# Optimization experiments

Measured on AMD Instinct MI355X. Metric: run time of the kernel, lower is better.

## Reference

```python
import jax, jax.numpy as jnp
import numpy as np

NUM_EXPERTS = 8
TOP_K = 2

def setup_inputs() -> dict:
    key = jax.random.key(0)
    ks = jax.random.split(key, 6)
    B, S, D, F, E = 2, 2048, 1024, 4096, NUM_EXPERTS
    scale = 0.02
    return {
        "x": jax.random.normal(ks[0], (B, S, D), dtype=jnp.float32),
        "router_w": jax.random.normal(ks[1], (E, D), dtype=jnp.float32) * scale,
        "router_b": jnp.zeros((E,), dtype=jnp.float32),
        "w1": jax.random.normal(ks[2], (E, D, F), dtype=jnp.float32) * scale,
        "w2": jax.random.normal(ks[3], (E, F, D), dtype=jnp.float32) * scale,
        "w3": jax.random.normal(ks[4], (E, D, F), dtype=jnp.float32) * scale,
    }

def reference(x, router_w, router_b, w1, w2, w3):
    B, S, D = x.shape
    E = router_w.shape[0]
    xf = x.reshape(-1, D)                                   # [T, D]
    logits = xf @ router_w.T + router_b                     # [T, E]
    probs = jax.nn.softmax(logits, axis=-1)
    topk_w, topk_idx = jax.lax.top_k(probs, TOP_K)          # [T, K]
    topk_w = topk_w / jnp.sum(topk_w, axis=-1, keepdims=True)
    # combine[t, e] = renormalized routing weight of expert e for token t (0 if not selected)
    combine = jnp.sum(jax.nn.one_hot(topk_idx, E, dtype=xf.dtype) * topk_w[..., None], axis=1)  # [T, E]
    out = jnp.zeros_like(xf)
    for e in range(E):  # small fixed expert count; each iter is a dense SwiGLU GEMM
        h = jax.nn.silu(xf @ w1[e]) * (xf @ w3[e])          # [T, F]
        out = out + combine[:, e:e + 1] * (h @ w2[e])       # [T, D]
    return out.reshape(B, S, D)
```

## Files before the change

kernel.cpp:

```cpp
#include <hip/hip_runtime.h>

typedef unsigned short ushort_t;
typedef __attribute__((ext_vector_type(8))) short short8;
typedef __attribute__((ext_vector_type(4))) float floatx4;

#define GAS __attribute__((address_space(1)))
#define LAS __attribute__((address_space(3)))

__device__ __forceinline__ float bf2f(ushort_t h) {
  union { unsigned int u; float f; } v; v.u = ((unsigned int)h) << 16; return v.f;
}
__device__ __forceinline__ ushort_t f2bf(float f) {
  union { float f; unsigned int u; } v; v.f = f;
  unsigned int u = v.u;
  unsigned int r = (u + 0x7fffu + ((u >> 16) & 1u)) >> 16;
  return (ushort_t)r;
}
__device__ __forceinline__ float blo(unsigned int u) { union { unsigned int u; float f; } v; v.u = u << 16; return v.f; }
__device__ __forceinline__ float bhi(unsigned int u) { union { unsigned int u; float f; } v; v.u = u & 0xffff0000u; return v.f; }

#define T_TOK 4096
#define DIM   1024
#define FDIM  4096
#define NEXP  8
#define MAXROWS 9216

__global__ void detect_kernel(const ushort_t* __restrict__ xraw, int* __restrict__ dflag) {
  __shared__ int cnt;
  if (threadIdx.x == 0) cnt = 0;
  __syncthreads();
  int c = 0;
#pragma unroll
  for (int i = 0; i < 4; ++i) {
    ushort_t u = xraw[(threadIdx.x * 4 + i) * 2];
    int e = (u >> 7) & 0xFF;
    if (e >= 100 && e <= 140) c++;
  }
  atomicAdd(&cnt, c);
  __syncthreads();
  if (threadIdx.x == 0) dflag[0] = (cnt > 600) ? 0 : 1;
}

__global__ void __launch_bounds__(256) castx_kernel(const void* __restrict__ xraw,
                                                    const int* __restrict__ dflag,
                                                    ushort_t* __restrict__ xb) {
  const int t = blockIdx.x * 256 + threadIdx.x;
  const size_t base = (size_t)t * 8;
  if (dflag[0]) {
    const float4* f = (const float4*)((const float*)xraw + base);
    float4 a = f[0], b = f[1];
    ushort_t o[8] = { f2bf(a.x), f2bf(a.y), f2bf(a.z), f2bf(a.w),
                      f2bf(b.x), f2bf(b.y), f2bf(b.z), f2bf(b.w) };
    *(uint4*)(xb + base) = *(const uint4*)o;
  } else {
    *(uint4*)(xb + base) = *((const uint4*)xraw + t);
  }
}

__global__ void __launch_bounds__(256) router_kernel(
    const void* __restrict__ x_, const ushort_t* __restrict__ xb,
    const void* __restrict__ rw_, const void* __restrict__ rb_,
    const int* __restrict__ dflag,
    int* __restrict__ topk_idx, float* __restrict__ topk_wgt, int* __restrict__ counts) {
  const int lane = threadIdx.x & 63;
  const int w = threadIdx.x >> 6;
  const int t = blockIdx.x * 4 + w;
  const int isf32 = dflag[0];
  double logits[NEXP];
  if (isf32) {
    const float* xr = (const float*)x_ + (size_t)t * DIM;
    float xv[16];
#pragma unroll
    for (int i = 0; i < 8; ++i) {
      const float2 v = *(const float2*)(xr + i * 128 + lane * 2);
      xv[2*i] = v.x; xv[2*i+1] = v.y;
    }
#pragma unroll
    for (int e = 0; e < NEXP; ++e) {
      const float* wr = (const float*)rw_ + (size_t)e * DIM;
      double acc = 0.0;
#pragma unroll
      for (int i = 0; i < 8; ++i) {
        const float2 v = *(const float2*)(wr + i * 128 + lane * 2);
        acc += (double)xv[2*i] * (double)v.x + (double)xv[2*i+1] * (double)v.y;
      }
#pragma unroll
      for (int off = 32; off > 0; off >>= 1) acc += __shfl_xor(acc, off, 64);
      logits[e] = acc + (double)((const float*)rb_)[e];
    }
  } else {
    const ushort_t* xr = xb + (size_t)t * DIM;
    float xv[16];
#pragma unroll
    for (int i = 0; i < 8; ++i) {
      unsigned int u = *(const unsigned int*)(xr + i * 128 + lane * 2);
      xv[2*i] = blo(u); xv[2*i+1] = bhi(u);
    }
#pragma unroll
    for (int e = 0; e < NEXP; ++e) {
      const ushort_t* wr = (const ushort_t*)rw_ + (size_t)e * DIM;
      float acc = 0.f;
#pragma unroll
      for (int i = 0; i < 8; ++i) {
        unsigned int u = *(const unsigned int*)(wr + i * 128 + lane * 2);
        acc += xv[2*i] * blo(u) + xv[2*i+1] * bhi(u);
      }
#pragma unroll
      for (int off = 32; off > 0; off >>= 1) acc += __shfl_xor(acc, off, 64);
      logits[e] = (double)(acc + bf2f(((const ushort_t*)rb_)[e]));
    }
  }
  if (lane == 0) {
    double l1 = -1e300, l2 = -1e300; int i1 = 0, i2 = 0;
#pragma unroll
    for (int e = 0; e < NEXP; ++e) {
      double l = logits[e];
      if (l > l1) { l2 = l1; i2 = i1; l1 = l; i1 = e; }
      else if (l > l2) { l2 = l; i2 = e; }
    }
    float wa = (float)(1.0 / (1.0 + exp(l2 - l1)));
    topk_idx[2*t] = i1; topk_idx[2*t+1] = i2;
    topk_wgt[2*t] = wa; topk_wgt[2*t+1] = 1.f - wa;
    atomicAdd(&counts[i1], 1);
    atomicAdd(&counts[i2], 1);
  }
}

__global__ void scan_kernel(const int* __restrict__ counts, int* __restrict__ offsets) {
  if (threadIdx.x == 0 && blockIdx.x == 0) {
    int s = 0; offsets[0] = 0;
    for (int e = 0; e < NEXP; ++e) { s += (counts[e] + 127) & ~127; offsets[e + 1] = s; }
  }
}

__global__ void __launch_bounds__(256) scatter_kernel(
    const int* __restrict__ topk_idx, const float* __restrict__ topk_wgt,
    const int* __restrict__ offsets, int* __restrict__ cursors,
    int* __restrict__ row_tok, float* __restrict__ row_wgt) {
  int p = blockIdx.x * 256 + threadIdx.x;
  int e = topk_idx[p];
  int pos = atomicAdd(&cursors[e], 1);
  int r = offsets[e] + pos;
  row_tok[r] = p >> 1;
  row_wgt[r] = topk_wgt[p];
}

__global__ void __launch_bounds__(256) transpose_kernel(
    const void* __restrict__ src_, ushort_t* __restrict__ dst, int R, int C,
    const int* __restrict__ dflag) {
  __shared__ unsigned int tile[64][33];
  const int e = blockIdx.z;
  const int r0 = blockIdx.y * 64;
  const int c0 = blockIdx.x * 64;
  const int tx = threadIdx.x;
  if (dflag[0]) {
    const float* S = (const float*)src_ + (size_t)e * R * C;
#pragma unroll
    for (int it = 0; it < 8; ++it) {
      int slot = tx + it * 256;
      int r = slot >> 5;
      int c2 = slot & 31;
      const float2 v = *(const float2*)(S + (size_t)(r0 + r) * C + c0 + c2 * 2);
      tile[r][c2] = (unsigned int)f2bf(v.x) | ((unsigned int)f2bf(v.y) << 16);
    }
  } else {
    const ushort_t* S = (const ushort_t*)src_ + (size_t)e * R * C;
#pragma unroll
    for (int it = 0; it < 2; ++it) {
      int slot = tx + it * 256;
      int r = slot >> 3;
      int cc = slot & 7;
      const uint4 v = *(const uint4*)(S + (size_t)(r0 + r) * C + c0 + cc * 8);
      tile[r][cc*4+0] = v.x; tile[r][cc*4+1] = v.y; tile[r][cc*4+2] = v.z; tile[r][cc*4+3] = v.w;
    }
  }
  __syncthreads();
#pragma unroll
  for (int it = 0; it < 2; ++it) {
    int slot = tx + it * 256;
    int c = slot >> 3;
    int rr = (slot & 7) * 8;
    unsigned int o[4];
#pragma unroll
    for (int q = 0; q < 4; ++q) {
      unsigned int a = tile[rr + 2*q][c >> 1];
      unsigned int b = tile[rr + 2*q + 1][c >> 1];
      unsigned int ha = (c & 1) ? (a >> 16) : (a & 0xffffu);
      unsigned int hb = (c & 1) ? (b >> 16) : (b & 0xffffu);
      o[q] = ha | (hb << 16);
    }
    *(uint4*)(dst + (size_t)e * R * C + (size_t)(c0 + c) * R + r0 + rr) = *(const uint4*)o;
  }
}

__device__ __forceinline__ int swz(int r) { return (r >> 1) & 3; }

__device__ __forceinline__ short8 frag_ld(const short* tile, int row, int q) {
  return *(const short8*)(tile + row * 32 + ((q ^ swz(row)) << 3));
}

__device__ __forceinline__ int chunk_expert(const int* offsets, int r0) {
  int e = 0;
  while (offsets[e + 1] <= r0) ++e;
  return e;
}

__global__ void __launch_bounds__(256) gemm1_kernel(
    const ushort_t* __restrict__ xb, const ushort_t* __restrict__ w1t, const ushort_t* __restrict__ w3t,
    const int* __restrict__ offsets, const int* __restrict__ row_tok, ushort_t* __restrict__ H) {
  const int r0 = blockIdx.y * 128;
  if (r0 >= offsets[NEXP]) return;
  const int e = chunk_expert(offsets, r0);
  const int fbase = blockIdx.x * 128;
  const ushort_t* w1e = w1t + (size_t)e * FDIM * DIM;
  const ushort_t* w3e = w3t + (size_t)e * FDIM * DIM;

  __shared__ __align__(16) short As[2][4096];
  __shared__ __align__(16) short B1s[2][4096];
  __shared__ __align__(16) short B3s[2][4096];

  const int lane = threadIdx.x & 63;
  const int wid = threadIdx.x >> 6;
  const int wrow = (wid >> 1) * 64;
  const int wcol = (wid & 1) * 64;
  const int l15 = lane & 15;
  const int quad = lane >> 4;

  const ushort_t* aP[2];  const ushort_t* b1P[2];  const ushort_t* b3P[2];
  int ldst[2];
#pragma unroll
  for (int tl = 0; tl < 2; ++tl) {
    const int tr0 = wid * 32 + tl * 16;
    const int r = tr0 + (lane >> 2);
    const int g = ((lane & 3) ^ swz(r)) * 8;
    aP[tl]  = xb  + (size_t)row_tok[r0 + r] * DIM + g;
    b1P[tl] = w1e + (size_t)(fbase + r) * DIM + g;
    b3P[tl] = w3e + (size_t)(fbase + r) * DIM + g;
    ldst[tl] = tr0 * 32;
  }

  floatx4 acc1[4][4], acc3[4][4];
  const floatx4 z4 = {0.f, 0.f, 0.f, 0.f};
#pragma unroll
  for (int i = 0; i < 4; ++i)
#pragma unroll
    for (int j = 0; j < 4; ++j) { acc1[i][j] = z4; acc3[i][j] = z4; }

  auto stage = [&](int k0, int buf) {
#pragma unroll
    for (int tl = 0; tl < 2; ++tl) {
      __builtin_amdgcn_global_load_lds((const GAS void*)(aP[tl]  + k0), (LAS void*)(&As[buf][ldst[tl]]),  16, 0, 0);
      __builtin_amdgcn_global_load_lds((const GAS void*)(b1P[tl] + k0), (LAS void*)(&B1s[buf][ldst[tl]]), 16, 0, 0);
      __builtin_amdgcn_global_load_lds((const GAS void*)(b3P[tl] + k0), (LAS void*)(&B3s[buf][ldst[tl]]), 16, 0, 0);
    }
  };
  auto compute = [&](int buf) {
    short8 a[4], b1[4], b3[4];
#pragma unroll
    for (int i = 0; i < 4; ++i) a[i] = frag_ld(&As[buf][0], wrow + i * 16 + l15, quad);
#pragma unroll
    for (int j = 0; j < 4; ++j) {
      b1[j] = frag_ld(&B1s[buf][0], wcol + j * 16 + l15, quad);
      b3[j] = frag_ld(&B3s[buf][0], wcol + j * 16 + l15, quad);
    }
#pragma unroll
    for (int i = 0; i < 4; ++i)
#pragma unroll
      for (int j = 0; j < 4; ++j) {
        acc1[i][j] = __builtin_amdgcn_mfma_f32_16x16x32_bf16(a[i], b1[j], acc1[i][j], 0, 0, 0);
        acc3[i][j] = __builtin_amdgcn_mfma_f32_16x16x32_bf16(a[i], b3[j], acc3[i][j], 0, 0, 0);
      }
  };

  stage(0, 0);
  __syncthreads();
  int cur = 0;
  for (int t = 0; t < DIM / 32 - 1; ++t) {
    stage((t + 1) * 32, cur ^ 1);
    compute(cur);
    __syncthreads();
    cur ^= 1;
  }
  compute(cur);

#pragma unroll
  for (int i = 0; i < 4; ++i)
#pragma unroll
    for (int j = 0; j < 4; ++j) {
      const int n = fbase + wcol + j * 16 + l15;
#pragma unroll
      for (int p = 0; p < 4; ++p) {
        const int rl = wrow + i * 16 + quad * 4 + p;
        float zt = acc1[i][j][p];
        float vt = acc3[i][j][p];
        float s = zt / (1.f + __expf(-zt));
        H[(size_t)(r0 + rl) * FDIM + n] = f2bf(s * vt);
      }
    }
}

__global__ void __launch_bounds__(256) gemm2_kernel(
    const ushort_t* __restrict__ H, const ushort_t* __restrict__ w2t,
    const int* __restrict__ offsets, const int* __restrict__ row_tok,
    const float* __restrict__ row_wgt, float* __restrict__ out) {
  const int r0 = blockIdx.y * 128;
  if (r0 >= offsets[NEXP]) return;
  const int e = chunk_expert(offsets, r0);
  const int dbase = blockIdx.x * 128;
  const ushort_t* w2e = w2t + (size_t)e * DIM * FDIM;

  __shared__ __align__(16) short As[2][4096];
  __shared__ __align__(16) short Bs[2][4096];

  const int lane = threadIdx.x & 63;
  const int wid = threadIdx.x >> 6;
  const int wrow = (wid >> 1) * 64;
  const int wcol = (wid & 1) * 64;
  const int l15 = lane & 15;
  const int quad = lane >> 4;

  const ushort_t* aP[2];  const ushort_t* bP[2];
  int ldst[2];
#pragma unroll
  for (int tl = 0; tl < 2; ++tl) {
    const int tr0 = wid * 32 + tl * 16;
    const int r = tr0 + (lane >> 2);
    const int g = ((lane & 3) ^ swz(r)) * 8;
    aP[tl] = H   + (size_t)(r0 + r) * FDIM + g;
    bP[tl] = w2e + (size_t)(dbase + r) * FDIM + g;
    ldst[tl] = tr0 * 32;
  }

  floatx4 acc[4][4];
  const floatx4 z4 = {0.f, 0.f, 0.f, 0.f};
#pragma unroll
  for (int i = 0; i < 4; ++i)
#pragma unroll
    for (int j = 0; j < 4; ++j) acc[i][j] = z4;

  auto stage = [&](int k0, int buf) {
#pragma unroll
    for (int tl = 0; tl < 2; ++tl) {
      __builtin_amdgcn_global_load_lds((const GAS void*)(aP[tl] + k0), (LAS void*)(&As[buf][ldst[tl]]), 16, 0, 0);
      __builtin_amdgcn_global_load_lds((const GAS void*)(bP[tl] + k0), (LAS void*)(&Bs[buf][ldst[tl]]), 16, 0, 0);
    }
  };
  auto compute = [&](int buf) {
    short8 a[4], b[4];
#pragma unroll
    for (int i = 0; i < 4; ++i) a[i] = frag_ld(&As[buf][0], wrow + i * 16 + l15, quad);
#pragma unroll
    for (int j = 0; j < 4; ++j) b[j] = frag_ld(&Bs[buf][0], wcol + j * 16 + l15, quad);
#pragma unroll
    for (int i = 0; i < 4; ++i)
#pragma unroll
      for (int j = 0; j < 4; ++j)
        acc[i][j] = __builtin_amdgcn_mfma_f32_16x16x32_bf16(a[i], b[j], acc[i][j], 0, 0, 0);
  };

  stage(0, 0);
  __syncthreads();
  int cur = 0;
  for (int t = 0; t < FDIM / 32 - 1; ++t) {
    stage((t + 1) * 32, cur ^ 1);
    compute(cur);
    __syncthreads();
    cur ^= 1;
  }
  compute(cur);

#pragma unroll
  for (int i = 0; i < 4; ++i) {
    int tok[4]; float wgt[4];
#pragma unroll
    for (int p = 0; p < 4; ++p) {
      int rl = r0 + wrow + i * 16 + quad * 4 + p;
      tok[p] = row_tok[rl];
      wgt[p] = row_wgt[rl];
    }
#pragma unroll
    for (int j = 0; j < 4; ++j) {
      int n = dbase + wcol + j * 16 + l15;
#pragma unroll
      for (int p = 0; p < 4; ++p)
        if (wgt[p] != 0.f)
          atomicAdd(&out[(size_t)tok[p] * DIM + n], wgt[p] * acc[i][j][p]);
    }
  }
}

extern "C" void kernel_launch(void* const* d_in, const int* in_sizes, int n_in,
                              void* d_out, int out_size, void* d_ws, size_t ws_size,
                              hipStream_t stream) {
  const void* x  = d_in[0];
  const void* rw = d_in[1];
  const void* rb = d_in[2];
  const void* w1 = d_in[3];
  const void* w2 = d_in[4];
  const void* w3 = d_in[5];
  float* out = (float*)d_out;

  char* ws = (char*)d_ws;
  size_t off = 0;
  auto alloc = [&](size_t bytes) { size_t o = off; off += (bytes + 255) & ~(size_t)255; return o; };
  int*      dflag    = (int*)(ws + alloc(64));
  int*      counts   = (int*)(ws + alloc(64));
  int*      cursors  = (int*)(ws + alloc(64));
  int*      offsets  = (int*)(ws + alloc(64));
  int*      topk_idx = (int*)(ws + alloc((size_t)T_TOK * 2 * 4));
  float*    topk_wgt = (float*)(ws + alloc((size_t)T_TOK * 2 * 4));
  int*      row_tok  = (int*)(ws + alloc((size_t)MAXROWS * 4));
  float*    row_wgt  = (float*)(ws + alloc((size_t)MAXROWS * 4));
  ushort_t* xb       = (ushort_t*)(ws + alloc((size_t)T_TOK * DIM * 2));
  ushort_t* Hbuf     = (ushort_t*)(ws + alloc((size_t)MAXROWS * FDIM * 2));
  ushort_t* w1t      = (ushort_t*)(ws + alloc((size_t)NEXP * FDIM * DIM * 2));
  ushort_t* w3t      = (ushort_t*)(ws + alloc((size_t)NEXP * FDIM * DIM * 2));
  ushort_t* w2t      = (ushort_t*)(ws + alloc((size_t)NEXP * DIM * FDIM * 2));

  hipMemsetAsync(counts, 0, 64, stream);
  hipMemsetAsync(cursors, 0, 64, stream);
  hipMemsetAsync(row_tok, 0, (size_t)MAXROWS * 4, stream);
  hipMemsetAsync(row_wgt, 0, (size_t)MAXROWS * 4, stream);
  hipMemsetAsync(out, 0, (size_t)out_size, stream);

  detect_kernel<<<1, 256, 0, stream>>>((const ushort_t*)x, dflag);
  castx_kernel<<<(T_TOK * DIM / 8) / 256, 256, 0, stream>>>(x, dflag, xb);
  router_kernel<<<T_TOK / 4, 256, 0, stream>>>(x, xb, rw, rb, dflag, topk_idx, topk_wgt, counts);
  scan_kernel<<<1, 64, 0, stream>>>(counts, offsets);
  scatter_kernel<<<(T_TOK * 2) / 256, 256, 0, stream>>>(topk_idx, topk_wgt, offsets, cursors, row_tok, row_wgt);
  transpose_kernel<<<dim3(FDIM / 64, DIM / 64, NEXP), 256, 0, stream>>>(w1, w1t, DIM, FDIM, dflag);
  transpose_kernel<<<dim3(FDIM / 64, DIM / 64, NEXP), 256, 0, stream>>>(w3, w3t, DIM, FDIM, dflag);
  transpose_kernel<<<dim3(DIM / 64, FDIM / 64, NEXP), 256, 0, stream>>>(w2, w2t, FDIM, DIM, dflag);
  gemm1_kernel<<<dim3(FDIM / 128, MAXROWS / 128), 256, 0, stream>>>(xb, w1t, w3t, offsets, row_tok, Hbuf);
  gemm2_kernel<<<dim3(DIM / 128, MAXROWS / 128), 256, 0, stream>>>(Hbuf, w2t, offsets, row_tok, row_wgt, out);
}
```

Baseline: 968.4 us.

## Triple-buffer LDS staging with explicit vmcnt waits in both expert GEMMs

Both grouped GEMM kernels move from double-buffered to triple-buffered shared-memory staging, prefetching two K-tiles ahead. Explicit s_waitcnt vmcnt counts replace __syncthreads, so each step waits only for the oldest tile's direct-to-LDS loads. This is meant to hide more global-load latency behind MFMA work. In exchange, LDS use grows (gemm1 to 72KB), which may lower occupancy, and correctness depends on the hand-counted vmcnt values matching the number of loads issued per stage.

```diff
diff --git a/kernel.cpp b/kernel.cpp
--- a/kernel.cpp
+++ b/kernel.cpp
@@ -215,9 +215,9 @@
   const ushort_t* w1e = w1t + (size_t)e * FDIM * DIM;
   const ushort_t* w3e = w3t + (size_t)e * FDIM * DIM;
 
-  __shared__ __align__(16) short As[2][4096];
-  __shared__ __align__(16) short B1s[2][4096];
-  __shared__ __align__(16) short B3s[2][4096];
+  __shared__ __align__(16) short As[3][4096];
+  __shared__ __align__(16) short B1s[3][4096];
+  __shared__ __align__(16) short B3s[3][4096];
 
   const int lane = threadIdx.x & 63;
   const int wid = threadIdx.x >> 6;
@@ -272,16 +272,24 @@
       }
   };
 
+  const int T = DIM / 32;
   stage(0, 0);
-  __syncthreads();
-  int cur = 0;
-  for (int t = 0; t < DIM / 32 - 1; ++t) {
-    stage((t + 1) * 32, cur ^ 1);
-    compute(cur);
-    __syncthreads();
-    cur ^= 1;
-  }
-  compute(cur);
+  stage(32, 1);
+  for (int t = 0; t < T; ++t) {
+    if (t + 2 < T) {
+      stage((t + 2) * 32, (t + 2) % 3);
+      asm volatile("s_waitcnt vmcnt(12)" ::: "memory");
+    } else if (t + 1 < T) {
+      asm volatile("s_waitcnt vmcnt(6)" ::: "memory");
+    } else {
+      asm volatile("s_waitcnt vmcnt(0)" ::: "memory");
+    }
+    __builtin_amdgcn_sched_barrier(0);
+    __builtin_amdgcn_s_barrier();
+    compute(t % 3);
+    __builtin_amdgcn_sched_barrier(0);
+    __builtin_amdgcn_s_barrier();
+  }
 
 #pragma unroll
   for (int i = 0; i < 4; ++i)
@@ -309,8 +317,8 @@
   const int dbase = blockIdx.x * 128;
   const ushort_t* w2e = w2t + (size_t)e * DIM * FDIM;
 
-  __shared__ __align__(16) short As[2][4096];
-  __shared__ __align__(16) short Bs[2][4096];
+  __shared__ __align__(16) short As[3][4096];
+  __shared__ __align__(16) short Bs[3][4096];
 
   const int lane = threadIdx.x & 63;
   const int wid = threadIdx.x >> 6;
@@ -358,16 +366,24 @@
         acc[i][j] = __builtin_amdgcn_mfma_f32_16x16x32_bf16(a[i], b[j], acc[i][j], 0, 0, 0);
   };
 
+  const int T = FDIM / 32;
   stage(0, 0);
-  __syncthreads();
-  int cur = 0;
-  for (int t = 0; t < FDIM / 32 - 1; ++t) {
-    stage((t + 1) * 32, cur ^ 1);
-    compute(cur);
-    __syncthreads();
-    cur ^= 1;
-  }
-  compute(cur);
+  stage(32, 1);
+  for (int t = 0; t < T; ++t) {
+    if (t + 2 < T) {
+      stage((t + 2) * 32, (t + 2) % 3);
+      asm volatile("s_waitcnt vmcnt(8)" ::: "memory");
+    } else if (t + 1 < T) {
+      asm volatile("s_waitcnt vmcnt(4)" ::: "memory");
+    } else {
+      asm volatile("s_waitcnt vmcnt(0)" ::: "memory");
+    }
+    __builtin_amdgcn_sched_barrier(0);
+    __builtin_amdgcn_s_barrier();
+    compute(t % 3);
+    __builtin_amdgcn_sched_barrier(0);
+    __builtin_amdgcn_s_barrier();
+  }
 
 #pragma unroll
   for (int i = 0; i < 4; ++i) {
```

Result: slower. 1.081 ms (+11.6%).
